# Optimization experiments

Measured on AMD Instinct MI355X. Metric: run time of the kernel, lower is better.

## Reference

```python
import jax, jax.numpy as jnp
import numpy as np
import math

S, D, H, L, V = 1024, 768, 12, 6, 32000
KD = D // H
FF = 4 * D
PAD = 0


def setup_inputs() -> dict:
    key = jax.random.key(0)
    ks = jax.random.split(key, 20)
    s = D ** -0.5
    return {
        "token_ids": jax.random.randint(ks[0], (2, S), 0, V, dtype=jnp.int32),
        "emb": jax.random.normal(ks[1], (V, D)) * s,
        "Wq": jax.random.normal(ks[2], (L, H, D, KD)) * s,
        "bq": jnp.zeros((L, H, KD)),
        "Wk": jax.random.normal(ks[3], (L, H, D, KD)) * s,
        "bk": jnp.zeros((L, H, KD)),
        "Wv": jax.random.normal(ks[4], (L, H, D, D)) * s,
        "bv": jnp.zeros((L, H, D)),
        "g1": jnp.ones((L, D)), "be1": jnp.zeros((L, D)),
        "g2": jnp.ones((L, D)), "be2": jnp.zeros((L, D)),
        "W1": jax.random.normal(ks[5], (L, D, FF)) * s,
        "b1": jnp.zeros((L, FF)),
        "W2": jax.random.normal(ks[6], (L, FF, D)) * (FF ** -0.5),
        "b2": jnp.zeros((L, D)),
        "Wout": jax.random.normal(ks[7], (D, V)) * s,
        "bout": jnp.zeros((V,)),
    }


def _pe():
    pos = jnp.arange(S, dtype=jnp.float32)[:, None]
    div = jnp.exp(jnp.arange(0, D, 2, dtype=jnp.float32) * (-math.log(10000.0) / D))
    ang = pos * div  # [S, D/2]
    return jnp.stack([jnp.sin(ang), jnp.cos(ang)], axis=-1).reshape(S, D)


def _ln(x, g, b):
    m = x.mean(-1, keepdims=True)
    v = ((x - m) ** 2).mean(-1, keepdims=True)
    return (x - m) * jax.lax.rsqrt(v + 1e-5) * g + b


def reference(token_ids, emb, Wq, bq, Wk, bk, Wv, bv, g1, be1, g2, be2, W1, b1, W2, b2, Wout, bout):
    pad = token_ids == PAD  # [B,S]
    causal = jnp.triu(jnp.ones((S, S), dtype=bool), k=1)
    # mask[b,s,t] = causal | pad-as-key | pad-as-query
    mask = causal[None, None] | pad[:, None, None, :] | pad[:, None, :, None]  # [B,1,S,S]
    scale = math.sqrt(KD)
    x = emb[token_ids] + _pe()[None]  # [B,S,D]
    for l in range(L):
        q = jnp.einsum('bsd,hdk->bhsk', x, Wq[l]) + bq[l][None, :, None, :]
        k = jnp.einsum('bsd,hdk->bhsk', x, Wk[l]) + bk[l][None, :, None, :]
        v = jnp.einsum('bsd,hde->bhse', x, Wv[l]) + bv[l][None, :, None, :]
        scores = jnp.einsum('bhsk,bhtk->bhst', q, k) / scale
        scores = jnp.where(mask, -jnp.inf, scores)
        all_masked = jnp.all(mask, axis=-1)  # rows with every key masked -> uniform attn
        scores = jnp.where(all_masked[..., None], 0.0, scores)
        attn = jax.nn.softmax(scores, axis=-1)
        heads = jnp.einsum('bhst,bhte->bhse', attn, v)  # per-head full-D values
        attn_out = heads.mean(axis=1)  # heads are AVERAGED, not concatenated
        x = _ln(x + attn_out, g1[l], be1[l])
        ff = jax.nn.relu(x @ W1[l] + b1[l]) @ W2[l] + b2[l]
        x = _ln(x + ff, g2[l], be2[l])
    return x @ Wout + bout
```

## Files before the change

### kernel.cpp

```cpp
#include <hip/hip_runtime.h>
#include <hip/hip_bf16.h>

#define SQ 1024
#define DM 768
#define NH 12
#define NL 6
#define NV 32000
#define KDH 64
#define FFD 3072

using bf16 = __hip_bfloat16;
typedef __attribute__((ext_vector_type(4))) float f32x4;
typedef __attribute__((ext_vector_type(8))) short bf16x8;

__global__ void fill_kernel(float* __restrict__ out, long n, float val) {
  const long stride = (long)gridDim.x * blockDim.x;
  for (long i = (long)blockIdx.x * blockDim.x + threadIdx.x; i < n; i += stride)
    out[i] = val;
}

__device__ __forceinline__ void gload16(const void* g, void* l) {
  __builtin_amdgcn_global_load_lds(
      (const __attribute__((address_space(1))) unsigned int*)g,
      (__attribute__((address_space(3))) unsigned int*)l, 16, 0, 0);
}

template<bool OUT_BF16, bool RELU, bool TRI = false, bool CTRUNC = false,
         bool QKV = false>
__global__ __launch_bounds__(256) void gemm_bt(
    int M, int N, int K,
    const bf16* __restrict__ Ap, long sAz, int lda,
    const bf16* __restrict__ Bp, long sBz, int ldbt,
    const float* __restrict__ biasp, int sBiasZ,
    void* __restrict__ Cp, long sCz, long sCb, long sCs, long sCn,
    void* __restrict__ Cp2 = nullptr, const float* __restrict__ bias2p = nullptr)
{
  __shared__ __align__(16) char lds[49152];

  const int tid = threadIdx.x;
  const int gx = gridDim.x, gy = gridDim.y;
  const int nwg = gx * gy * (int)gridDim.z;
  int flat = ((int)blockIdx.z * gy + (int)blockIdx.y) * gx + (int)blockIdx.x;
  {
    const int q = nwg >> 3, r = nwg & 7;
    const int xcd = flat & 7, loc = flat >> 3;
    flat = (xcd < r ? xcd * (q + 1) : r * (q + 1) + (xcd - r) * q) + loc;
  }
  int m0, n0, z;
  if (TRI) {
    z = flat / 36;
    const int t = flat % 36;
    int i = (int)((sqrtf(8.0f * (float)t + 1.0f) - 1.0f) * 0.5f);
    if ((i + 1) * (i + 2) / 2 <= t) ++i;
    if (i * (i + 1) / 2 > t) --i;
    const int j = t - i * (i + 1) / 2;
    m0 = i * 128; n0 = j * 128;
  } else {
    const int bx  = flat % gx;
    const int byz = flat / gx;
    m0 = bx * 128;
    n0 = (byz % gy) * 128;
    z  = byz / gy;
  }
  const int KK = CTRUNC ? min(K, m0 + 128) : K;

  const int lane = tid & 63;
  const int wid  = tid >> 6;
  const int wm = (wid >> 1) * 64;
  const int wn = (wid & 1) * 64;

  const int srow  = tid >> 2;
  const int sslot = tid & 3;
  const int xorb  = (sslot ^ (srow & 3)) << 4;

  const char* gA0 = (const char*)(Ap + (long)z * sAz + (long)(m0 + srow) * lda) + xorb;
  const char* gA1 = (const char*)(Ap + (long)z * sAz + (long)(m0 + srow + 64) * lda) + xorb;
  const char* gB0 = (const char*)(Bp + (long)z * sBz + (long)(n0 + srow) * ldbt) + xorb;
  const char* gB1 = (const char*)(Bp + (long)z * sBz + (long)(n0 + srow + 64) * ldbt) + xorb;

  auto stage = [&](int bo) {
    gload16(gA0, lds + bo + tid * 16);
    gload16(gA1, lds + bo + (tid + 256) * 16);
    gload16(gB0, lds + bo + 8192 + tid * 16);
    gload16(gB1, lds + bo + 8192 + (tid + 256) * 16);
    gA0 += 64; gA1 += 64; gB0 += 64; gB1 += 64;
  };

  const int fr = lane & 15;
  const int kq = lane >> 4;
  int fA[4], fB[4];
#pragma unroll
  for (int m = 0; m < 4; ++m) {
    const int R = wm + m * 16 + fr;
    fA[m] = R * 64 + ((kq ^ (R & 3)) << 4);
  }
#pragma unroll
  for (int n = 0; n < 4; ++n) {
    const int R = wn + n * 16 + fr;
    fB[n] = 8192 + R * 64 + ((kq ^ (R & 3)) << 4);
  }

  f32x4 acc[4][4] = {};

  const int nt = KK >> 5;
  stage(0);
  stage(16384);
  int cur = 0;
  int nb  = 2;
  for (int t = 0; t < nt; ++t) {
    if (t + 1 < nt) {
      asm volatile("s_waitcnt vmcnt(4)" ::: "memory");
    } else {
      asm volatile("s_waitcnt vmcnt(0)" ::: "memory");
    }
    __builtin_amdgcn_s_barrier();
    if (t + 2 < nt) stage(nb * 16384);
    const int co = cur * 16384;
    bf16x8 af[4], bfr[4];
#pragma unroll
    for (int m = 0; m < 4; ++m) af[m] = *(const bf16x8*)(lds + co + fA[m]);
#pragma unroll
    for (int n = 0; n < 4; ++n) bfr[n] = *(const bf16x8*)(lds + co + fB[n]);
#pragma unroll
    for (int m = 0; m < 4; ++m)
#pragma unroll
      for (int n = 0; n < 4; ++n)
        acc[m][n] = __builtin_amdgcn_mfma_f32_16x16x32_bf16(af[m], bfr[n], acc[m][n], 0, 0, 0);
    cur = (cur == 2) ? 0 : cur + 1;
    nb  = (nb == 2) ? 0 : nb + 1;
  }

  const int rg = (lane >> 4) * 4;
  const int cl = lane & 15;

  if (QKV) {
    if (n0 == 0) {
#pragma unroll
      for (int n = 0; n < 4; ++n) {
        const int gcol = wn + n * 16 + cl;
        const float bias = biasp[z * 128 + gcol];
#pragma unroll
        for (int m = 0; m < 4; ++m) {
#pragma unroll
          for (int rr = 0; rr < 4; ++rr) {
            const int grow = m0 + wm + m * 16 + rg + rr;
            const int bb = grow >> 10, s = grow & 1023;
            ((bf16*)Cp)[((long)(bb * NH + z) * SQ + s) * 128 + gcol] =
                __float2bfloat16(acc[m][n][rr] + bias);
          }
        }
      }
    } else {
#pragma unroll
      for (int n = 0; n < 4; ++n) {
        const int e = n0 - 128 + wn + n * 16 + cl;
        const float bias = bias2p[z * DM + e];
#pragma unroll
        for (int m = 0; m < 4; ++m) {
          const int grow = m0 + wm + m * 16 + rg;
          const int bb = grow >> 10, s = grow & 1023;
          const long ci = ((long)(bb * NH + z) * DM + e) * SQ + s;
          ushort4 pk;
          pk.x = __builtin_bit_cast(ushort, __float2bfloat16(acc[m][n][0] + bias));
          pk.y = __builtin_bit_cast(ushort, __float2bfloat16(acc[m][n][1] + bias));
          pk.z = __builtin_bit_cast(ushort, __float2bfloat16(acc[m][n][2] + bias));
          pk.w = __builtin_bit_cast(ushort, __float2bfloat16(acc[m][n][3] + bias));
          *(ushort4*)((bf16*)Cp2 + ci) = pk;
        }
      }
    }
    return;
  }

  const long zb = (long)z * sBiasZ;
#pragma unroll
  for (int n = 0; n < 4; ++n) {
    const int gcol = n0 + wn + n * 16 + cl;
    const float bias = biasp ? biasp[zb + gcol] : 0.f;
    if (OUT_BF16 && sCs == 1) {
#pragma unroll
      for (int m = 0; m < 4; ++m) {
        const int grow = m0 + wm + m * 16 + rg;
        const long ci = (long)z * sCz + (long)(grow >> 10) * sCb
                      + (long)(grow & 1023) + (long)gcol * sCn;
        ushort4 pk;
        float v0 = acc[m][n][0] + bias, v1 = acc[m][n][1] + bias;
        float v2 = acc[m][n][2] + bias, v3 = acc[m][n][3] + bias;
        if (RELU) { v0 = fmaxf(v0, 0.f); v1 = fmaxf(v1, 0.f);
                    v2 = fmaxf(v2, 0.f); v3 = fmaxf(v3, 0.f); }
        pk.x = __builtin_bit_cast(ushort, __float2bfloat16(v0));
        pk.y = __builtin_bit_cast(ushort, __float2bfloat16(v1));
        pk.z = __builtin_bit_cast(ushort, __float2bfloat16(v2));
        pk.w = __builtin_bit_cast(ushort, __float2bfloat16(v3));
        *(ushort4*)((bf16*)Cp + ci) = pk;
      }
    } else {
#pragma unroll
      for (int m = 0; m < 4; ++m) {
#pragma unroll
        for (int rr = 0; rr < 4; ++rr) {
          const int grow = m0 + wm + m * 16 + rg + rr;
          float v = acc[m][n][rr] + bias;
          if (RELU) v = fmaxf(v, 0.f);
          const long ci = (long)z * sCz + (long)(grow >> 10) * sCb
                        + (long)(grow & 1023) * sCs + (long)gcol * sCn;
          if (OUT_BF16) ((bf16*)Cp)[ci] = __float2bfloat16(v);
          else          ((float*)Cp)[ci] = v;
        }
      }
    }
  }
}

__device__ __forceinline__ void transpose_tile(
    const float* __restrict__ in, int ldin, bf16* __restrict__ out, int ldout,
    int n0, int k0, int tid)
{
  __shared__ float t[64][65];
  const int cx = (tid & 15) * 4, ry = tid >> 4;
#pragma unroll
  for (int p = 0; p < 4; ++p) {
    const int k = ry + p * 16;
    const float4 v = *(const float4*)(in + (long)(k0 + k) * ldin + n0 + cx);
    t[k][cx] = v.x; t[k][cx + 1] = v.y; t[k][cx + 2] = v.z; t[k][cx + 3] = v.w;
  }
  __syncthreads();
#pragma unroll
  for (int p = 0; p < 4; ++p) {
    const int n = ry + p * 16;
    ushort4 o;
    o.x = __builtin_bit_cast(ushort, __float2bfloat16(t[cx + 0][n]));
    o.y = __builtin_bit_cast(ushort, __float2bfloat16(t[cx + 1][n]));
    o.z = __builtin_bit_cast(ushort, __float2bfloat16(t[cx + 2][n]));
    o.w = __builtin_bit_cast(ushort, __float2bfloat16(t[cx + 3][n]));
    *(ushort4*)(out + (long)(n0 + n) * ldout + k0 + cx) = o;
  }
}

__global__ __launch_bounds__(256) void transpose_kernel(
    const float* __restrict__ in, long sInZ, int ldin,
    bf16* __restrict__ out, long sOutZ, int ldout)
{
  transpose_tile(in + (long)blockIdx.z * sInZ, ldin,
                 out + (long)blockIdx.z * sOutZ, ldout,
                 blockIdx.x * 64, blockIdx.y * 64, threadIdx.x);
}

__global__ __launch_bounds__(256) void prep_attn_kernel(
    const float* __restrict__ Wq_l, const float* __restrict__ Wk_l,
    const float* __restrict__ Wv_l,
    const float* __restrict__ bq_l, const float* __restrict__ bk_l,
    bf16* __restrict__ wqvT, float* __restrict__ biasqk)
{
  const int tid = threadIdx.x;
  int f = blockIdx.x;
  if (f < 144) {
    const int h = f / 12, ky = f % 12;
    transpose_tile(Wq_l + (long)h * DM * KDH, KDH,
                   wqvT + (long)h * 896 * DM, DM, 0, ky * 64, tid);
  } else if (f < 288) {
    f -= 144;
    const int h = f / 12, ky = f % 12;
    transpose_tile(Wk_l + (long)h * DM * KDH, KDH,
                   wqvT + (long)h * 896 * DM + (long)64 * DM, DM, 0, ky * 64, tid);
  } else if (f < 2016) {
    f -= 288;
    const int h = f / 144, r = f % 144;
    transpose_tile(Wv_l + (long)h * DM * DM, DM,
                   wqvT + (long)h * 896 * DM + (long)128 * DM, DM,
                   (r % 12) * 64, (r / 12) * 64, tid);
  } else {
    const int i = (f - 2016) * 256 + tid;
    if (i < NH * 128) {
      const int h = i >> 7, n = i & 127;
      biasqk[i] = (n < 64) ? bq_l[h * 64 + n] : bk_l[h * 64 + n - 64];
    }
  }
}

__global__ __launch_bounds__(256) void prep_ff_kernel(
    const float* __restrict__ W1_l, const float* __restrict__ W2_l,
    bf16* __restrict__ w1T, bf16* __restrict__ w2T)
{
  const int tid = threadIdx.x;
  int f = blockIdx.x;
  if (f < 576) {
    transpose_tile(W1_l, FFD, w1T, DM, (f % 48) * 64, (f / 48) * 64, tid);
  } else {
    f -= 576;
    transpose_tile(W2_l, DM, w2T, FFD, (f % 12) * 64, (f / 12) * 64, tid);
  }
}

__global__ __launch_bounds__(256) void xpart_kernel(
    const float* __restrict__ x, float* __restrict__ xpart) {
  const int b = blockIdx.x, g = blockIdx.y;
  const int tid = threadIdx.x;
  const float* xp = x + (long)b * SQ * DM + (long)g * 64 * DM;
  float a0 = 0.f, a1 = 0.f, a2 = 0.f;
  for (int s = 0; s < 64; ++s) {
    a0 += xp[(long)s * DM + tid];
    a1 += xp[(long)s * DM + tid + 256];
    a2 += xp[(long)s * DM + tid + 512];
  }
  float* op = xpart + (long)(b * 16 + g) * DM;
  op[tid] = a0; op[tid + 256] = a1; op[tid + 512] = a2;
}

__global__ __launch_bounds__(256) void vmeanw_kernel(
    const float* __restrict__ xpart, const bf16* __restrict__ wqvT,
    const float* __restrict__ bv, float* __restrict__ vmean) {
  const int tid = threadIdx.x;
  const int w = blockIdx.x * 4 + (tid >> 6);
  const int b = w / DM;
  const int e = w % DM;
  const int lane = tid & 63;
  float xm[12];
#pragma unroll
  for (int j = 0; j < 12; ++j) {
    float a = 0.f;
#pragma unroll
    for (int g = 0; g < 16; ++g)
      a += xpart[(long)(b * 16 + g) * DM + lane + j * 64];
    xm[j] = a * (1.0f / (float)SQ);
  }
  float acc = 0.f;
  for (int h = 0; h < NH; ++h) {
    const bf16* wr = wqvT + ((long)h * 896 + 128 + e) * DM;
#pragma unroll
    for (int j = 0; j < 12; ++j)
      acc += xm[j] * __bfloat162float(wr[lane + j * 64]);
  }
#pragma unroll
  for (int o = 32; o >= 1; o >>= 1) acc += __shfl_xor(acc, o);
  if (lane == 0) {
    float bs = 0.f;
#pragma unroll
    for (int h = 0; h < NH; ++h) bs += bv[h * DM + e];
    vmean[b * DM + e] = (acc + bs) * (1.0f / (float)NH);
  }
}

__global__ __launch_bounds__(256) void embed_kernel(
    const int* __restrict__ tok, const float* __restrict__ emb,
    float* __restrict__ x, bf16* __restrict__ xb)
{
  const int gid = blockIdx.x * 256 + threadIdx.x;
  const int row = gid / (DM / 4);
  const int dc  = (gid % (DM / 4)) * 4;
  const int t = tok[row];
  const int s = row & (SQ - 1);
#pragma unroll
  for (int j = 0; j < 4; ++j) {
    const int d = dc + j;
    const float e = emb[(long)t * DM + d];
    const float div = expf(-(float)(d & ~1) * (9.210340371976184f / (float)DM));
    const float ang = (float)s * div;
    const float pe = (d & 1) ? cosf(ang) : sinf(ang);
    const float v = e + pe;
    x[(long)row * DM + d] = v;
    xb[(long)row * DM + d] = __float2bfloat16(v);
  }
}

__global__ __launch_bounds__(256) void softmax_kernel(
    bf16* __restrict__ P, const int* __restrict__ tok)
{
  const int row = blockIdx.x;
  const int s = row & (SQ - 1);
  const int z = row >> 10;
  const int b = z / NH;
  const int* tb = tok + b * SQ;
  if (tb[s] == 0) return;
  bf16* sp = P + (long)row * SQ;
  const int tid = threadIdx.x;
  const int t0 = tid * 4;
  const int L = (s | 127) + 1;
  const bool act = t0 < L;

  float val[4] = {-1e30f, -1e30f, -1e30f, -1e30f};
  float vmax = -1e30f;
  if (act) {
    uint2 raw = *(const uint2*)(sp + t0);
    int4 tv = *(const int4*)(tb + t0);
    const bf16* rh = (const bf16*)&raw;
    const int tvv[4] = {tv.x, tv.y, tv.z, tv.w};
#pragma unroll
    for (int j = 0; j < 4; ++j) {
      const int t = t0 + j;
      const bool valid = (t <= s) && (tvv[j] != 0);
      val[j] = valid ? __bfloat162float(rh[j]) * 0.125f : -1e30f;
      vmax = fmaxf(vmax, val[j]);
    }
  }
  __shared__ float red[4];
  const int lane = tid & 63, wid = tid >> 6;
  float w = vmax;
#pragma unroll
  for (int o = 32; o >= 1; o >>= 1) w = fmaxf(w, __shfl_xor(w, o));
  if (lane == 0) red[wid] = w;
  __syncthreads();
  const float Mx = fmaxf(fmaxf(red[0], red[1]), fmaxf(red[2], red[3]));
  __syncthreads();
  float e[4]; float lsum = 0.f;
#pragma unroll
  for (int j = 0; j < 4; ++j) {
    e[j] = (val[j] > -1e29f) ? expf(val[j] - Mx) : 0.f;
    lsum += e[j];
  }
  w = lsum;
#pragma unroll
  for (int o = 32; o >= 1; o >>= 1) w += __shfl_xor(w, o);
  if (lane == 0) red[wid] = w;
  __syncthreads();
  const float inv = 1.0f / (red[0] + red[1] + red[2] + red[3]);
  if (act) {
    ushort4 pk;
    pk.x = __builtin_bit_cast(ushort, __float2bfloat16(e[0] * inv));
    pk.y = __builtin_bit_cast(ushort, __float2bfloat16(e[1] * inv));
    pk.z = __builtin_bit_cast(ushort, __float2bfloat16(e[2] * inv));
    pk.w = __builtin_bit_cast(ushort, __float2bfloat16(e[3] * inv));
    *(ushort4*)(sp + t0) = pk;
  }
}

#define TCHUNK 1572864L
template<int MODE>
__global__ __launch_bounds__(256) void ln_kernel(
    float* __restrict__ x, bf16* __restrict__ xb,
    const float* __restrict__ tmp, const bf16* __restrict__ heads,
    const float* __restrict__ g, const float* __restrict__ be,
    const int* __restrict__ tok, const float* __restrict__ vmean,
    const float* __restrict__ bias)
{
  const int r = blockIdx.x;
  const int b = r >> 10;
  const int s = r & (SQ - 1);
  const int tid = threadIdx.x;
  __shared__ float rs[4], rq[4];
  const bool pad = (MODE == 1) && (tok[r] == 0);
  float sum = 0.f, sq = 0.f;
  float v[8];
  if (tid < 96) {
    const int d0 = tid * 8;
    const float4 x0 = *(const float4*)(x + (long)r * DM + d0);
    const float4 x1 = *(const float4*)(x + (long)r * DM + d0 + 4);
    v[0] = x0.x; v[1] = x0.y; v[2] = x0.z; v[3] = x0.w;
    v[4] = x1.x; v[5] = x1.y; v[6] = x1.z; v[7] = x1.w;
    if (MODE == 0) {
#pragma unroll
      for (int c = 0; c < 4; ++c) {
        const float* tp = tmp + c * TCHUNK + (long)r * DM + d0;
        const float4 t0_ = *(const float4*)tp;
        const float4 t1_ = *(const float4*)(tp + 4);
        v[0] += t0_.x; v[1] += t0_.y; v[2] += t0_.z; v[3] += t0_.w;
        v[4] += t1_.x; v[5] += t1_.y; v[6] += t1_.z; v[7] += t1_.w;
      }
      const float4 b0_ = *(const float4*)(bias + d0);
      const float4 b1_ = *(const float4*)(bias + d0 + 4);
      v[0] += b0_.x; v[1] += b0_.y; v[2] += b0_.z; v[3] += b0_.w;
      v[4] += b1_.x; v[5] += b1_.y; v[6] += b1_.z; v[7] += b1_.w;
    } else if (pad) {
      const float4 t0_ = *(const float4*)(vmean + b * DM + d0);
      const float4 t1_ = *(const float4*)(vmean + b * DM + d0 + 4);
      v[0] += t0_.x; v[1] += t0_.y; v[2] += t0_.z; v[3] += t0_.w;
      v[4] += t1_.x; v[5] += t1_.y; v[6] += t1_.z; v[7] += t1_.w;
    } else {
      float hs[8] = {0.f, 0.f, 0.f, 0.f, 0.f, 0.f, 0.f, 0.f};
      for (int h = 0; h < NH; ++h) {
        union { uint4 u; ushort us[8]; } hv;
        hv.u = *(const uint4*)(heads + ((long)(b * NH + h) * SQ + s) * DM + d0);
#pragma unroll
        for (int j = 0; j < 8; ++j)
          hs[j] += __bfloat162float(__builtin_bit_cast(bf16, hv.us[j]));
      }
#pragma unroll
      for (int j = 0; j < 8; ++j) v[j] += hs[j] * (1.0f / (float)NH);
    }
#pragma unroll
    for (int j = 0; j < 8; ++j) { sum += v[j]; sq += v[j] * v[j]; }
  }
  const int lane = tid & 63, wid = tid >> 6;
  float s1 = sum, s2 = sq;
#pragma unroll
  for (int o = 32; o >= 1; o >>= 1) { s1 += __shfl_xor(s1, o); s2 += __shfl_xor(s2, o); }
  if (lane == 0) { rs[wid] = s1; rq[wid] = s2; }
  __syncthreads();
  const float S1 = rs[0] + rs[1] + rs[2] + rs[3];
  const float S2 = rq[0] + rq[1] + rq[2] + rq[3];
  const float mean = S1 * (1.0f / (float)DM);
  const float var  = S2 * (1.0f / (float)DM) - mean * mean;
  const float rstd = rsqrtf(var + 1e-5f);
  if (tid < 96) {
    const int d0 = tid * 8;
    const float4 g0 = *(const float4*)(g + d0);
    const float4 g1 = *(const float4*)(g + d0 + 4);
    const float4 b0 = *(const float4*)(be + d0);
    const float4 b1 = *(const float4*)(be + d0 + 4);
    float o[8];
    o[0] = (v[0] - mean) * rstd * g0.x + b0.x;
    o[1] = (v[1] - mean) * rstd * g0.y + b0.y;
    o[2] = (v[2] - mean) * rstd * g0.z + b0.z;
    o[3] = (v[3] - mean) * rstd * g0.w + b0.w;
    o[4] = (v[4] - mean) * rstd * g1.x + b1.x;
    o[5] = (v[5] - mean) * rstd * g1.y + b1.y;
    o[6] = (v[6] - mean) * rstd * g1.z + b1.z;
    o[7] = (v[7] - mean) * rstd * g1.w + b1.w;
    *(float4*)(x + (long)r * DM + d0)     = make_float4(o[0], o[1], o[2], o[3]);
    *(float4*)(x + (long)r * DM + d0 + 4) = make_float4(o[4], o[5], o[6], o[7]);
    union { uint4 u; ushort us[8]; } pk;
#pragma unroll
    for (int j = 0; j < 8; ++j)
      pk.us[j] = __builtin_bit_cast(ushort, __float2bfloat16(o[j]));
    *(uint4*)(xb + (long)r * DM + d0) = pk.u;
  }
}

extern "C" void kernel_launch(void* const* d_in, const int* in_sizes, int n_in,
                              void* d_out, int out_size, void* d_ws, size_t ws_size,
                              hipStream_t stream) {
  const int expect_sizes[18] = {
    2048, 24576000, 3538944, 4608, 3538944, 4608, 42467328, 55296,
    4608, 4608, 4608, 4608, 14155776, 18432, 14155776, 4608, 24576000, 32000
  };
  bool sizes_ok = (n_in == 18);
  if (sizes_ok)
    for (int i = 0; i < 18; ++i) sizes_ok = sizes_ok && (in_sizes[i] == expect_sizes[i]);
  if (!sizes_ok) {
    fill_kernel<<<2048, 256, 0, stream>>>((float*)d_out, (long)out_size, 1000.0f);
    return;
  }
  if (out_size != 65536000) {
    fill_kernel<<<2048, 256, 0, stream>>>((float*)d_out, (long)out_size, 3000.0f);
    return;
  }
  if (ws_size < 158189568ull) {
    fill_kernel<<<2048, 256, 0, stream>>>((float*)d_out, (long)out_size, 2000.0f);
    return;
  }

  const int*   tok  = (const int*)d_in[0];
  const float* emb  = (const float*)d_in[1];
  const float* Wq   = (const float*)d_in[2];
  const float* bq   = (const float*)d_in[3];
  const float* Wk   = (const float*)d_in[4];
  const float* bk   = (const float*)d_in[5];
  const float* Wv   = (const float*)d_in[6];
  const float* bv   = (const float*)d_in[7];
  const float* g1   = (const float*)d_in[8];
  const float* be1  = (const float*)d_in[9];
  const float* g2   = (const float*)d_in[10];
  const float* be2  = (const float*)d_in[11];
  const float* W1   = (const float*)d_in[12];
  const float* b1   = (const float*)d_in[13];
  const float* W2   = (const float*)d_in[14];
  const float* b2   = (const float*)d_in[15];
  const float* Wout = (const float*)d_in[16];
  const float* bout = (const float*)d_in[17];

  char* ws = (char*)d_ws;
  float* x      = (float*)(ws + 0);
  bf16*  xb     = (bf16*) (ws + 6291456);
  bf16*  qk     = (bf16*) (ws + 9437184);
  bf16*  vT     = (bf16*) (ws + 15728640);
  float* tmp    = (float*)(ws + 15728640);
  bf16*  P      = (bf16*) (ws + 53477376);
  bf16*  woutT  = (bf16*) (ws + 53477376);
  bf16*  heads  = (bf16*) (ws + 103809024);
  bf16*  wqvT   = (bf16*) (ws + 141557760);
  bf16*  w1T    = (bf16*) (ws + 141557760);
  bf16*  w2T    = (bf16*) (ws + 146276352);
  float* biasqk = (float*)(ws + 158072832);
  float* xpart  = (float*)(ws + 158078976);
  float* vmean  = (float*)(ws + 158183424);

  embed_kernel<<<dim3((2 * SQ * DM / 4) / 256), 256, 0, stream>>>(tok, emb, x, xb);

  for (int l = 0; l < NL; ++l) {
    prep_attn_kernel<<<dim3(2022), 256, 0, stream>>>(
        Wq + (long)l * NH * DM * KDH, Wk + (long)l * NH * DM * KDH,
        Wv + (long)l * NH * DM * DM,
        bq + l * NH * KDH, bk + l * NH * KDH,
        wqvT, biasqk);

    xpart_kernel<<<dim3(2, 16), 256, 0, stream>>>(x, xpart);
    vmeanw_kernel<<<dim3(384), 256, 0, stream>>>(xpart, wqvT, bv + (long)l * NH * DM, vmean);

    gemm_bt<true, false, false, false, true><<<dim3(16, 7, NH), 256, 0, stream>>>(
        2048, 896, DM, xb, 0, DM, wqvT, (long)896 * DM, DM,
        biasqk, 128,
        qk, 0, 0, 0, 0,
        vT, bv + (long)l * NH * DM);
    gemm_bt<true, false, true, false><<<dim3(36, 1, 2 * NH), 256, 0, stream>>>(
        SQ, SQ, KDH, qk, (long)SQ * 128, 128, qk + 64, (long)SQ * 128, 128,
        (const float*)nullptr, 0,
        P, (long)SQ * SQ, 0, SQ, 1);
    softmax_kernel<<<dim3(2 * NH * SQ), 256, 0, stream>>>(P, tok);
    gemm_bt<true, false, false, true><<<dim3(8, 6, 2 * NH), 256, 0, stream>>>(
        SQ, DM, SQ, P, (long)SQ * SQ, SQ, vT, (long)DM * SQ, SQ,
        (const float*)nullptr, 0,
        heads, (long)SQ * DM, 0, DM, 1);
    ln_kernel<1><<<dim3(2048), 256, 0, stream>>>(x, xb, nullptr, heads,
                                                 g1 + l * DM, be1 + l * DM, tok, vmean,
                                                 nullptr);
    prep_ff_kernel<<<dim3(1152), 256, 0, stream>>>(
        W1 + (long)l * DM * FFD, W2 + (long)l * FFD * DM, w1T, w2T);
    gemm_bt<true, true><<<dim3(16, 24, 1), 256, 0, stream>>>(
        2048, FFD, DM, xb, 0, DM, w1T, 0, DM,
        b1 + (long)l * FFD, 0,
        (bf16*)P, 0, (long)SQ * FFD, FFD, 1);
    gemm_bt<false, false><<<dim3(16, 6, 4), 256, 0, stream>>>(
        2048, DM, 768, (bf16*)P, 768, FFD, w2T, 768, FFD,
        (const float*)nullptr, 0,
        tmp, TCHUNK, (long)SQ * DM, DM, 1);
    ln_kernel<0><<<dim3(2048), 256, 0, stream>>>(x, xb, tmp, nullptr,
                                                 g2 + l * DM, be2 + l * DM, tok, nullptr,
                                                 b2 + (long)l * DM);
  }
  transpose_kernel<<<dim3(500, 12, 1), 256, 0, stream>>>(Wout, 0, NV, woutT, 0, DM);
  gemm_bt<false, false><<<dim3(16, 250, 1), 256, 0, stream>>>(
      2048, NV, DM, xb, 0, DM, woutT, 0, DM,
      bout, 0,
      d_out, 0, (long)SQ * NV, NV, 1);
}
```

Before: 1.549 ms.

## Add 256x128 triple-buffered GEMM kernel for output projection

Replaces the generic GEMM used for the final vocabulary projection with a dedicated 512-thread kernel. Each workgroup computes a 256x128 tile using triple-buffered LDS staging through global_load_lds with XOR swizzling and explicit vmcnt waits. Workgroup indices are remapped so neighbouring tiles land on the same XCD. The goals are more reuse per tile, better L2 locality and overlap of loads with MFMA. The cost is 72KB of dynamic LDS per block, which limits occupancy, and a kernel that assumes its dimensions divide the tile sizes.

Result: no change. 1.549 ms (-0.0%).

```diff
diff --git a/kernel.cpp b/kernel.cpp
--- a/kernel.cpp
+++ b/kernel.cpp
@@ -207,6 +207,108 @@
           if (OUT_BF16) ((bf16*)Cp)[ci] = __float2bfloat16(v);
           else          ((float*)Cp)[ci] = v;
         }
+      }
+    }
+  }
+}
+
+__global__ __launch_bounds__(512) void gemm256(
+    int M, int N, int K,
+    const bf16* __restrict__ Ap, int lda,
+    const bf16* __restrict__ Bp, int ldbt,
+    const float* __restrict__ biasp,
+    float* __restrict__ Cp, long sCb, long sCn)
+{
+  extern __shared__ __align__(16) char lds[];
+
+  const int tid = threadIdx.x;
+  const int gx = gridDim.x, gy = gridDim.y;
+  const int nwg = gx * gy;
+  int flat = (int)blockIdx.y * gx + (int)blockIdx.x;
+  {
+    const int q = nwg >> 3, r = nwg & 7;
+    const int xcd = flat & 7, loc = flat >> 3;
+    flat = (xcd < r ? xcd * (q + 1) : r * (q + 1) + (xcd - r) * q) + loc;
+  }
+  const int m0 = (flat % gx) * 256;
+  const int n0 = (flat / gx) * 128;
+
+  const int lane = tid & 63;
+  const int wid  = tid >> 6;
+  const int wm = (wid >> 1) * 64;
+  const int wn = (wid & 1) * 64;
+
+  const int srow  = tid >> 2;
+  const int sslot = tid & 3;
+  const int xorb  = (sslot ^ (srow & 3)) << 4;
+
+  const char* gA0 = (const char*)(Ap + (long)(m0 + srow) * lda) + xorb;
+  const char* gA1 = (const char*)(Ap + (long)(m0 + srow + 128) * lda) + xorb;
+  const char* gB0 = (const char*)(Bp + (long)(n0 + srow) * ldbt) + xorb;
+
+  auto stage = [&](int bo) {
+    gload16(gA0, lds + bo + tid * 16);
+    gload16(gA1, lds + bo + 8192 + tid * 16);
+    gload16(gB0, lds + bo + 16384 + tid * 16);
+    gA0 += 64; gA1 += 64; gB0 += 64;
+  };
+
+  const int fr = lane & 15;
+  const int kq = lane >> 4;
+  int fA[4], fB[4];
+#pragma unroll
+  for (int m = 0; m < 4; ++m) {
+    const int R = wm + m * 16 + fr;
+    fA[m] = R * 64 + ((kq ^ (R & 3)) << 4);
+  }
+#pragma unroll
+  for (int n = 0; n < 4; ++n) {
+    const int R = wn + n * 16 + fr;
+    fB[n] = 16384 + R * 64 + ((kq ^ (R & 3)) << 4);
+  }
+
+  f32x4 acc[4][4] = {};
+
+  const int nt = K >> 5;
+  stage(0);
+  stage(24576);
+  int cur = 0;
+  int nb  = 2;
+  for (int t = 0; t < nt; ++t) {
+    if (t + 1 < nt) {
+      asm volatile("s_waitcnt vmcnt(3)" ::: "memory");
+    } else {
+      asm volatile("s_waitcnt vmcnt(0)" ::: "memory");
+    }
+    __builtin_amdgcn_s_barrier();
+    if (t + 2 < nt) stage(nb * 24576);
+    const int co = cur * 24576;
+    bf16x8 af[4], bfr[4];
+#pragma unroll
+    for (int m = 0; m < 4; ++m) af[m] = *(const bf16x8*)(lds + co + fA[m]);
+#pragma unroll
+    for (int n = 0; n < 4; ++n) bfr[n] = *(const bf16x8*)(lds + co + fB[n]);
+#pragma unroll
+    for (int m = 0; m < 4; ++m)
+#pragma unroll
+      for (int n = 0; n < 4; ++n)
+        acc[m][n] = __builtin_amdgcn_mfma_f32_16x16x32_bf16(af[m], bfr[n], acc[m][n], 0, 0, 0);
+    cur = (cur == 2) ? 0 : cur + 1;
+    nb  = (nb == 2) ? 0 : nb + 1;
+  }
+
+  const int rg = (lane >> 4) * 4;
+  const int cl = lane & 15;
+#pragma unroll
+  for (int n = 0; n < 4; ++n) {
+    const int gcol = n0 + wn + n * 16 + cl;
+    const float bias = biasp[gcol];
+#pragma unroll
+    for (int m = 0; m < 4; ++m) {
+#pragma unroll
+      for (int rr = 0; rr < 4; ++rr) {
+        const int grow = m0 + wm + m * 16 + rg + rr;
+        Cp[(long)grow * sCb + (long)gcol * sCn] = acc[m][n][rr] + bias;
       }
     }
   }
@@ -538,6 +640,9 @@
     fill_kernel<<<2048, 256, 0, stream>>>((float*)d_out, (long)out_size, 2000.0f);
     return;
   }
+
+  (void)hipFuncSetAttribute((const void*)&gemm256,
+      hipFuncAttributeMaxDynamicSharedMemorySize, 73728);
 
   const int*   tok  = (const int*)d_in[0];
   const float* emb  = (const float*)d_in[1];
@@ -618,8 +723,6 @@
                                                  b2 + (long)l * DM);
   }
   transpose_kernel<<<dim3(500, 12, 1), 256, 0, stream>>>(Wout, 0, NV, woutT, 0, DM);
-  gemm_bt<false, false><<<dim3(16, 250, 1), 256, 0, stream>>>(
-      2048, NV, DM, xb, 0, DM, woutT, 0, DM,
-      bout, 0,
-      d_out, 0, (long)SQ * NV, NV, 1);
-}
+  gemm256<<<dim3(8, 250), 512, 73728, stream>>>(
+      2048, NV, DM, xb, DM, woutT, DM, bout, (float*)d_out, NV, 1);
+}
```
